# Kernel optimization log

Measured on AMD Instinct MI355X. Metric: run time of the kernel, lower is better.

## Reference

```python
import jax, jax.numpy as jnp
import numpy as np

HS = 1024          # hidden_size
NH_ATTN = 16       # attention heads
NH_LACT = 4        # lact fast-weight heads
DIN = HS // NH_LACT  # 256
DH = DIN             # inter_multi = 1
CHUNK = 1024       # lact_chunk_size
EPS = 1e-5


def setup_inputs() -> dict:
    key = jax.random.key(0)
    ks = jax.random.split(key, 6)
    B, S = 1, 4096
    x = jax.random.normal(ks[0], (B, S, HS), jnp.float32)
    ln_w = jnp.ones((HS,), jnp.float32)
    ln_b = jnp.zeros((HS,), jnp.float32)
    in_proj_w = jax.random.normal(ks[1], (3 * HS, HS), jnp.float32) * (HS ** -0.5)
    in_proj_b = jnp.zeros((3 * HS,), jnp.float32)
    out_proj_w = jax.random.normal(ks[2], (HS, HS), jnp.float32) * (HS ** -0.5)
    out_proj_b = jnp.zeros((HS,), jnp.float32)
    w0 = jax.random.normal(ks[3], (NH_LACT, DH, DIN), jnp.float32) / np.sqrt(DIN)
    w1 = jax.random.normal(ks[4], (NH_LACT, DIN, DH), jnp.float32) / np.sqrt(DH)
    w2 = jax.random.normal(ks[5], (NH_LACT, DH, DIN), jnp.float32) / np.sqrt(DIN)
    return dict(x=x, ln_w=ln_w, ln_b=ln_b, in_proj_w=in_proj_w, in_proj_b=in_proj_b,
                out_proj_w=out_proj_w, out_proj_b=out_proj_b, w0=w0, w1=w1, w2=w2)


def reference(x, ln_w, ln_b, in_proj_w, in_proj_b, out_proj_w, out_proj_b, w0, w1, w2):
    B, S, D = x.shape
    # LayerNorm
    mu = jnp.mean(x, axis=-1, keepdims=True)
    var = jnp.var(x, axis=-1, keepdims=True)
    xn = (x - mu) * jax.lax.rsqrt(var + EPS) * ln_w + ln_b

    # --- torch nn.MultiheadAttention(batch_first=True), self-attention, no mask ---
    qkv = xn @ in_proj_w.T + in_proj_b                      # [B,S,3D]
    q, k, v = jnp.split(qkv, 3, axis=-1)
    hd = D // NH_ATTN
    def heads(t):
        return t.reshape(B, S, NH_ATTN, hd).transpose(0, 2, 1, 3)  # [B,H,S,hd]
    q = heads(q) * (hd ** -0.5)
    k = heads(k)
    v = heads(v)
    attn = jax.nn.softmax(jnp.einsum('bhqd,bhkd->bhqk', q, k), axis=-1)
    ao = jnp.einsum('bhqk,bhkd->bhqd', attn, v).transpose(0, 2, 1, 3).reshape(B, S, D)
    attn_out = ao @ out_proj_w.T + out_proj_b

    # --- chunked fast-weight SwiGLU TTT (block_causal_lact_swiglu) ---
    # q=k=v=chunk; lr0=lr1=lr2=1; each outer chunk is one TTT step starting from
    # the module parameters: update weights on (k,v) then apply to q (block-causal).
    nc = S // CHUNK
    c = xn.reshape(B, nc, CHUNK, NH_LACT, DIN).transpose(0, 1, 3, 2, 4)  # [B,nc,nh,C,din]
    kv = c  # k == v == q == chunk

    # fast-weight SwiGLU forward on keys: f(k) = w1 @ (silu(w0 k) * (w2 k))
    gate = jnp.einsum('bnhcd,hed->bnhce', kv, w0)     # [B,nc,nh,C,dh]
    sg = jax.nn.sigmoid(gate)
    h = gate * sg                                     # silu
    g = jnp.einsum('bnhcd,hed->bnhce', kv, w2)
    hidden = h * g

    # negative dot-product loss L = -sum(v * f(k)) -> dOut = -v
    dout = -kv                                        # [B,nc,nh,C,din]
    dhid = jnp.einsum('bnhcd,hde->bnhce', dout, w1)
    dh = dhid * g
    dg = dhid * h
    dpre = dh * (sg + gate * sg * (1.0 - sg))         # silu'
    dw1 = jnp.einsum('bnhcd,bnhce->bnhde', dout, hidden)
    dw0 = jnp.einsum('bnhce,bnhcd->bnhed', dpre, kv)
    dw2 = jnp.einsum('bnhce,bnhcd->bnhed', dg, kv)

    # SGD step (lr = 1)
    w0n = w0 - dw0   # [B,nc,nh,dh,din]
    w1n = w1 - dw1
    w2n = w2 - dw2

    # apply updated fast weights to queries
    gq = jnp.einsum('bnhcd,bnhed->bnhce', c, w0n)
    hq = gq * jax.nn.sigmoid(gq)
    gq2 = jnp.einsum('bnhcd,bnhed->bnhce', c, w2n)
    oq = jnp.einsum('bnhce,bnhde->bnhcd', hq * gq2, w1n)  # [B,nc,nh,C,din]
    lact_out = oq.transpose(0, 1, 3, 2, 4).reshape(B, S, D)

    return lact_out + attn_out
```

## Files before the change

### kernel.cpp

```cpp
#include <hip/hip_runtime.h>
#include <hip/hip_bf16.h>


typedef __bf16 bf16_t;
typedef __bf16 bf16x8 __attribute__((ext_vector_type(8)));
typedef __bf16 bf16x4 __attribute__((ext_vector_type(4)));
typedef float  f32x4  __attribute__((ext_vector_type(4)));
typedef float  f32x16 __attribute__((ext_vector_type(16)));

#define SW64(r,cg) ((cg) ^ ((r)&7))
#define SW32(r,cg) ((cg) ^ (((r)>>2)&3))

static __device__ __forceinline__ f32x4 mfma16(bf16x8 a, bf16x8 b, f32x4 c){
  return __builtin_amdgcn_mfma_f32_16x16x32_bf16(a, b, c, 0, 0, 0);
}
static __device__ __forceinline__ f32x16 mfma32(bf16x8 a, bf16x8 b, f32x16 c){
  return __builtin_amdgcn_mfma_f32_32x32x16_bf16(a, b, c, 0, 0, 0);
}
__device__ __forceinline__ float sigm(float x){ return 1.0f/(1.0f + __expf(-x)); }
static __device__ __forceinline__ unsigned pkbf(float lo, float hi){
  unsigned short a = __builtin_bit_cast(unsigned short, (__bf16)lo);
  unsigned short b = __builtin_bit_cast(unsigned short, (__bf16)hi);
  return (unsigned)a | ((unsigned)b<<16);
}
static __device__ __forceinline__ float hswap_max(float x){
  float a=x, b=x;
  asm volatile("v_permlane32_swap_b32 %0, %1" : "+v"(a), "+v"(b));
  return fmaxf(a,b);
}
static __device__ __forceinline__ float hswap_add(float x){
  float a=x, b=x;
  asm volatile("v_permlane32_swap_b32 %0, %1" : "+v"(a), "+v"(b));
  return a+b;
}

__global__ __launch_bounds__(256) void ln_kernel(const float* __restrict__ x,
    const float* __restrict__ w, const float* __restrict__ b,
    bf16_t* __restrict__ xnb)
{
  int s = blockIdx.x, t = threadIdx.x;
  const float4* xr = (const float4*)(x + (size_t)s*1024);
  float4 v = xr[t];
  float sum = v.x+v.y+v.z+v.w;
  float ss  = v.x*v.x+v.y*v.y+v.z*v.z+v.w*v.w;
  #pragma unroll
  for (int o=32;o>0;o>>=1){ sum += __shfl_down(sum,o); ss += __shfl_down(ss,o); }
  __shared__ float red[8];
  __shared__ float stats[2];
  int wid=t>>6, lane=t&63;
  if(lane==0){ red[wid]=sum; red[4+wid]=ss; }
  __syncthreads();
  if(t==0){
    float S0=red[0]+red[1]+red[2]+red[3];
    float Q0=red[4]+red[5]+red[6]+red[7];
    float mu=S0*(1.0f/1024.0f);
    float var=Q0*(1.0f/1024.0f)-mu*mu;
    stats[0]=mu; stats[1]=rsqrtf(var+1e-5f);
  }
  __syncthreads();
  float mu=stats[0], rs=stats[1];
  float4 wv=((const float4*)w)[t], bv=((const float4*)b)[t];
  float4 o;
  o.x=(v.x-mu)*rs*wv.x+bv.x;
  o.y=(v.y-mu)*rs*wv.y+bv.y;
  o.z=(v.z-mu)*rs*wv.z+bv.z;
  o.w=(v.w-mu)*rs*wv.w+bv.w;
  bf16x4 ob = { (bf16_t)o.x, (bf16_t)o.y, (bf16_t)o.z, (bf16_t)o.w };
  *(bf16x4*)&xnb[(size_t)s*1024 + t*4] = ob;
}

__global__ __launch_bounds__(256) void prep_weights(
  const float* __restrict__ ipw, const float* __restrict__ opw,
  const float* __restrict__ w0, const float* __restrict__ w2,
  const float* __restrict__ w1,
  bf16_t* __restrict__ ipwb, bf16_t* __restrict__ opwb,
  bf16_t* __restrict__ w0b, bf16_t* __restrict__ w2b, bf16_t* __restrict__ w1tb)
{
  long i = ((long)blockIdx.x*256 + threadIdx.x)*4;
  if (i < 3145728) {
    float4 v = *(const float4*)(ipw + i);
    bf16x4 o = {(bf16_t)v.x,(bf16_t)v.y,(bf16_t)v.z,(bf16_t)v.w};
    *(bf16x4*)&ipwb[i] = o;
  } else if (i < 4194304) {
    long j = i - 3145728;
    float4 v = *(const float4*)(opw + j);
    bf16x4 o = {(bf16_t)v.x,(bf16_t)v.y,(bf16_t)v.z,(bf16_t)v.w};
    *(bf16x4*)&opwb[j] = o;
  } else if (i < 4456448) {
    long j = i - 4194304;
    float4 v = *(const float4*)(w0 + j);
    bf16x4 o = {(bf16_t)v.x,(bf16_t)v.y,(bf16_t)v.z,(bf16_t)v.w};
    *(bf16x4*)&w0b[j] = o;
  } else if (i < 4718592) {
    long j = i - 4456448;
    float4 v = *(const float4*)(w2 + j);
    bf16x4 o = {(bf16_t)v.x,(bf16_t)v.y,(bf16_t)v.z,(bf16_t)v.w};
    *(bf16x4*)&w2b[j] = o;
  } else if (i < 4980736) {
    long j = i - 4718592;
    int h = (int)(j>>16), rem = (int)(j&65535), d = rem>>8, e0 = rem&255;
    float4 v = *(const float4*)(w1 + j);
    bf16_t* dst = w1tb + h*65536 + d;
    dst[(e0+0)*256] = (bf16_t)v.x;
    dst[(e0+1)*256] = (bf16_t)v.y;
    dst[(e0+2)*256] = (bf16_t)v.z;
    dst[(e0+3)*256] = (bf16_t)v.w;
  }
}

__global__ __launch_bounds__(256) void xnT_kernel(const bf16_t* __restrict__ xnb,
                                                  bf16_t* __restrict__ xt)
{
  int dt = blockIdx.x, ct = blockIdx.y, bz = blockIdx.z;
  int nb = bz>>2, hb = bz&3;
  int t = threadIdx.x;
  __shared__ __align__(16) bf16_t T[4096];
  int r = t>>2, seg = t&3;
  const bf16_t* src = xnb + ((size_t)nb*1024 + ct*64 + r)*1024 + hb*256 + dt*64 + seg*16;
  uint4 a0 = *(const uint4*)src;
  uint4 a1 = *(const uint4*)(src + 8);
  *(uint4*)&T[r*64 + ((((seg*2  )&7)^(r&7))<<3)] = a0;
  *(uint4*)&T[r*64 + ((((seg*2+1)&7)^(r&7))<<3)] = a1;
  __syncthreads();
  int d = t>>2, s2 = t&3;
  unsigned uu[8];
  #pragma unroll
  for (int p=0;p<8;p++){
    int c0 = s2*16 + 2*p, c1 = c0+1;
    unsigned short e0 = __builtin_bit_cast(unsigned short,
        T[c0*64 + (((d>>3)^(c0&7))<<3) + (d&7)]);
    unsigned short e1 = __builtin_bit_cast(unsigned short,
        T[c1*64 + (((d>>3)^(c1&7))<<3) + (d&7)]);
    uu[p] = (unsigned)e0 | ((unsigned)e1<<16);
  }
  uint4 o0 = {uu[0],uu[1],uu[2],uu[3]}, o1 = {uu[4],uu[5],uu[6],uu[7]};
  bf16_t* dst = xt + (size_t)bz*262144 + (size_t)(dt*64 + d)*1024 + ct*64 + s2*16;
  *(uint4*)dst = o0;
  *(uint4*)(dst+8) = o1;
}

template<bool AEW>
__device__ __forceinline__ void gemm_core(
    const bf16_t* __restrict__ A, const float* __restrict__ F0,
    const float* __restrict__ F1, int lda,
    const bf16_t* __restrict__ B, int ldb,
    int K, int m0, int n0, f32x4 (&acc)[4][4])
{
  int t = threadIdx.x, l = t&63;
  int w = t>>6, wr = w>>1, wc = w&1;
  __shared__ __align__(16) bf16_t As[4096], Bs[4096];
  int r0 = t>>2, c0 = t&3, r1 = r0+64;
  const bf16_t* Arow0 = nullptr; const bf16_t* Arow1 = nullptr;
  const float *Fa0=nullptr,*Fa1=nullptr,*Fb0=nullptr,*Fb1=nullptr;
  if constexpr (AEW) {
    Fa0 = F0 + (size_t)(m0+r0)*lda + c0*8;
    Fa1 = F0 + (size_t)(m0+r1)*lda + c0*8;
    Fb0 = F1 + (size_t)(m0+r0)*lda + c0*8;
    Fb1 = F1 + (size_t)(m0+r1)*lda + c0*8;
  } else {
    Arow0 = A + (size_t)(m0+r0)*lda + c0*8;
    Arow1 = A + (size_t)(m0+r1)*lda + c0*8;
  }
  const bf16_t* Brow0 = B + (size_t)(n0+r0)*ldb + c0*8;
  const bf16_t* Brow1 = B + (size_t)(n0+r1)*ldb + c0*8;

  uint4 av0, av1, bv0, bv1;
  auto loadA = [&](int k0, uint4& o0, uint4& o1){
    if constexpr (AEW) {
      float4 ga = *(const float4*)(Fa0 + k0), gb = *(const float4*)(Fa0 + k0 + 4);
      float4 ha = *(const float4*)(Fb0 + k0), hb = *(const float4*)(Fb0 + k0 + 4);
      o0.x = pkbf(ga.x*sigm(ga.x)*ha.x, ga.y*sigm(ga.y)*ha.y);
      o0.y = pkbf(ga.z*sigm(ga.z)*ha.z, ga.w*sigm(ga.w)*ha.w);
      o0.z = pkbf(gb.x*sigm(gb.x)*hb.x, gb.y*sigm(gb.y)*hb.y);
      o0.w = pkbf(gb.z*sigm(gb.z)*hb.z, gb.w*sigm(gb.w)*hb.w);
      float4 gc = *(const float4*)(Fa1 + k0), gd = *(const float4*)(Fa1 + k0 + 4);
      float4 hc = *(const float4*)(Fb1 + k0), hd = *(const float4*)(Fb1 + k0 + 4);
      o1.x = pkbf(gc.x*sigm(gc.x)*hc.x, gc.y*sigm(gc.y)*hc.y);
      o1.y = pkbf(gc.z*sigm(gc.z)*hc.z, gc.w*sigm(gc.w)*hc.w);
      o1.z = pkbf(gd.x*sigm(gd.x)*hd.x, gd.y*sigm(gd.y)*hd.y);
      o1.w = pkbf(gd.z*sigm(gd.z)*hd.z, gd.w*sigm(gd.w)*hd.w);
    } else {
      o0 = *(const uint4*)(Arow0 + k0);
      o1 = *(const uint4*)(Arow1 + k0);
    }
  };
  loadA(0, av0, av1);
  bv0 = *(const uint4*)Brow0; bv1 = *(const uint4*)Brow1;
  int wo0 = r0*32 + (SW32(r0,c0)<<3), wo1 = r1*32 + (SW32(r1,c0)<<3);

  for (int k0=0; k0<K; k0+=32) {
    if (k0) __syncthreads();
    *(uint4*)&As[wo0] = av0; *(uint4*)&As[wo1] = av1;
    *(uint4*)&Bs[wo0] = bv0; *(uint4*)&Bs[wo1] = bv1;
    __syncthreads();
    if (k0+32 < K) {
      loadA(k0+32, av0, av1);
      bv0 = *(const uint4*)(Brow0 + k0+32); bv1 = *(const uint4*)(Brow1 + k0+32);
    }
    bf16x8 af[4], bb[4];
    #pragma unroll
    for (int mt=0;mt<4;mt++){
      int row = (wr<<6)+(mt<<4)+(l&15);
      af[mt] = *(bf16x8*)&As[row*32 + (SW32(row, (l>>4))<<3)];
    }
    #pragma unroll
    for (int nt=0;nt<4;nt++){
      int row = (wc<<6)+(nt<<4)+(l&15);
      bb[nt] = *(bf16x8*)&Bs[row*32 + (SW32(row, (l>>4))<<3)];
    }
    #pragma unroll
    for (int mt=0;mt<4;mt++)
      #pragma unroll
      for (int nt=0;nt<4;nt++)
        acc[mt][nt] = mfma16(af[mt], bb[nt], acc[mt][nt]);
  }
}

#define EPILOOP(...) { int l=threadIdx.x&63, w_=threadIdx.x>>6, wr=w_>>1, wc=w_&1; \
  _Pragma("unroll") for(int mt=0;mt<4;mt++) _Pragma("unroll") for(int nt=0;nt<4;nt++) \
  _Pragma("unroll") for(int q=0;q<4;q++){ \
    int gr=m0+(wr<<6)+(mt<<4)+((l>>4)<<2)+q; int gc=n0+(wc<<6)+(nt<<4)+(l&15); \
    float v=acc[mt][nt][q]; __VA_ARGS__ } }

#define ACCZERO f32x4 acc[4][4]; \
  _Pragma("unroll") for(int i_=0;i_<4;i_++) _Pragma("unroll") for(int j_=0;j_<4;j_++){ \
    f32x4 z_={0.f,0.f,0.f,0.f}; acc[i_][j_]=z_; }

template<int EPI>
__global__ __launch_bounds__(256) void gemm_big(
  const bf16_t* __restrict__ A, const bf16_t* __restrict__ B,
  float* __restrict__ C, const float* __restrict__ bias,
  bf16_t* __restrict__ O1, bf16_t* __restrict__ O2, bf16_t* __restrict__ O3,
  int K, int ldc)
{
  int m0 = blockIdx.y<<7, n0 = blockIdx.x<<7;
  ACCZERO
  gemm_core<false>(A, nullptr, nullptr, K, B, K, K, m0, n0, acc);
  EPILOOP(
    if constexpr (EPI==1) {
      C[(size_t)gr*ldc + gc] = v + bias[gc];
    } else {
      v += bias[gc];
      int seg = gc>>10; int c2 = gc&1023; int hh = c2>>6; int dd = c2&63;
      size_t oi = ((size_t)hh*4096 + gr)*64 + dd;
      if (seg==0)      O1[oi] = (bf16_t)(v*0.18033688011112042f);
      else if (seg==1) O2[oi] = (bf16_t)v;
      else             O3[oi] = (bf16_t)v;
    }
  )
}

__global__ __launch_bounds__(256) void lact_fwd(
    const bf16_t* __restrict__ xnb,
    const bf16_t* __restrict__ w0b, const bf16_t* __restrict__ w2b,
    const bf16_t* __restrict__ w1tb,
    float* __restrict__ b0, float* __restrict__ b1, float* __restrict__ b2)
{
  int bz = blockIdx.z, sel = blockIdx.x>>1;
  const bf16_t* A = xnb + (size_t)(bz>>2)*1048576 + (size_t)(bz&3)*256;
  const bf16_t* B = (sel==0?w0b:(sel==1?w2b:w1tb)) + (size_t)(bz&3)*65536;
  float* C = (sel==0?b0:(sel==1?b1:b2)) + (size_t)bz*262144;
  int m0 = blockIdx.y<<7, n0 = (blockIdx.x&1)<<7;
  ACCZERO
  gemm_core<false>(A, nullptr, nullptr, 1024, B, 256, 256, m0, n0, acc);
  EPILOOP( C[(size_t)gr*256 + gc] = v; )
}

__global__ __launch_bounds__(256) void lact_apply(
    const bf16_t* __restrict__ xnb,
    const bf16_t* __restrict__ w0nb, const bf16_t* __restrict__ w2nb,
    float* __restrict__ b0, float* __restrict__ b1)
{
  int bz = blockIdx.z, sel = blockIdx.x>>1;
  const bf16_t* A = xnb + (size_t)(bz>>2)*1048576 + (size_t)(bz&3)*256;
  const bf16_t* B = (sel? w2nb : w0nb) + (size_t)bz*65536;
  float* C = (sel? b1 : b0) + (size_t)bz*262144;
  int m0 = blockIdx.y<<7, n0 = (blockIdx.x&1)<<7;
  ACCZERO
  gemm_core<false>(A, nullptr, nullptr, 1024, B, 256, 256, m0, n0, acc);
  EPILOOP( C[(size_t)gr*256 + gc] = v; )
}

__global__ __launch_bounds__(256) void lact_upd(
    const bf16_t* __restrict__ xnTb, const bf16_t* __restrict__ hTb,
    const bf16_t* __restrict__ pTb,  const bf16_t* __restrict__ gTb,
    const float* __restrict__ w1, const float* __restrict__ w0,
    const float* __restrict__ w2,
    bf16_t* __restrict__ w1nb, bf16_t* __restrict__ w0nb, bf16_t* __restrict__ w2nb)
{
  int zz = blockIdx.z, sub = zz>>4, bz = zz&15, hb = bz&3;
  const bf16_t* A = (sub==0? xnTb : (sub==1? pTb : gTb)) + (size_t)bz*262144;
  const bf16_t* B = (sub==0? hTb : xnTb) + (size_t)bz*262144;
  const float*  P = (sub==0? w1 : (sub==1? w0 : w2)) + (size_t)hb*65536;
  bf16_t*       O = (sub==0? w1nb : (sub==1? w0nb : w2nb)) + (size_t)bz*65536;
  float sgn = (sub==0) ? 1.0f : -1.0f;
  int m0 = blockIdx.y<<7, n0 = blockIdx.x<<7;
  ACCZERO
  gemm_core<false>(A, nullptr, nullptr, 1024, B, 1024, 1024, m0, n0, acc);
  EPILOOP( O[(size_t)gr*256 + gc] = (bf16_t)(P[(size_t)gr*256 + gc] + sgn*v); )
}

__global__ __launch_bounds__(256) void lact_final(
    const float* __restrict__ gq, const float* __restrict__ gq2,
    const bf16_t* __restrict__ w1nb, float* __restrict__ out)
{
  int bz = blockIdx.z;
  const float* F0 = gq  + (size_t)bz*262144;
  const float* F1 = gq2 + (size_t)bz*262144;
  const bf16_t* B = w1nb + (size_t)bz*65536;
  float* C = out + (size_t)(bz>>2)*1048576 + (size_t)(bz&3)*256;
  int m0 = blockIdx.y<<7, n0 = (blockIdx.x&1)<<7;
  ACCZERO
  gemm_core<true>(nullptr, F0, F1, 256, B, 256, 256, m0, n0, acc);
  EPILOOP( C[(size_t)gr*1024 + gc] += v; )
}

__global__ __launch_bounds__(256) void vtrans(const bf16_t* __restrict__ Vb,
                                              bf16_t* __restrict__ Vt)
{
  int st = blockIdx.x, h = blockIdx.y, t = threadIdx.x;
  __shared__ __align__(16) bf16_t T[64*72];
  #pragma unroll
  for (int G=t; G<512; G+=256) {
    int r = G>>3, cg = G&7;
    *(uint4*)&T[r*72 + cg*8] =
      *(const uint4*)(Vb + ((size_t)h*4096 + st*64 + r)*64 + cg*8);
  }
  __syncthreads();
  int d = t>>2, seg = t&3;
  bf16x8 e0, e1;
  #pragma unroll
  for (int i=0;i<8;i++)  e0[i] = T[(seg*16+i)*72 + d];
  #pragma unroll
  for (int i=0;i<8;i++)  e1[i] = T[(seg*16+8+i)*72 + d];
  size_t base = ((size_t)h*64 + d)*4096 + st*64 + seg*16;
  *(bf16x8*)(Vt + base)     = e0;
  *(bf16x8*)(Vt + base + 8) = e1;
}

__global__ __launch_bounds__(256,4) void attn_mfma3(
    const bf16_t* __restrict__ Qb, const bf16_t* __restrict__ Kb,
    const bf16_t* __restrict__ Vt, float* __restrict__ Opart,
    float* __restrict__ mlpart)
{
  int h = blockIdx.x, qblk = blockIdx.y, z = blockIdx.z;
  int t = threadIdx.x, w = t>>6, l = t&63;
  int lh = l>>5, lq = l&31;
  __shared__ __align__(16) bf16_t Ks[4096], Vs[4096];

  const bf16_t* Kg = Kb + (size_t)h*262144 + (size_t)z*131072;
  const bf16_t* Vg = Vt + (size_t)h*262144 + (size_t)z*2048;

  bf16x8 qf[4];
  {
    const bf16_t* Qg = Qb + ((size_t)h*4096 + (size_t)qblk*128 + w*32 + lq)*64 + lh*8;
    #pragma unroll
    for (int s=0;s<4;s++) qf[s] = *(const bf16x8*)(Qg + s*16);
  }

  int r0 = t>>3, c0 = t&7, r1 = r0+32;
  uint4 kv0 = *(const uint4*)(Kg + (size_t)r0*64 + c0*8);
  uint4 kv1 = *(const uint4*)(Kg + (size_t)r1*64 + c0*8);
  uint4 vv0 = *(const uint4*)(Vg + (size_t)r0*4096 + c0*8);
  uint4 vv1 = *(const uint4*)(Vg + (size_t)r1*4096 + c0*8);

  float m_r = -1e30f, l_r = 0.f;
  f32x16 Oa, Ob;
  #pragma unroll
  for (int i=0;i<16;i++){ Oa[i]=0.f; Ob[i]=0.f; }

  int wo0 = r0*64 + (SW64(r0,c0)<<3);
  int wo1 = r1*64 + (SW64(r1,c0)<<3);

  for (int kt=0; kt<32; ++kt) {
    __syncthreads();
    *(uint4*)&Ks[wo0] = kv0;
    *(uint4*)&Ks[wo1] = kv1;
    *(uint4*)&Vs[wo0] = vv0;
    *(uint4*)&Vs[wo1] = vv1;
    __syncthreads();
    if (kt < 31) {
      const bf16_t* Kg2 = Kg + (size_t)(kt+1)*4096;
      kv0 = *(const uint4*)(Kg2 + (size_t)r0*64 + c0*8);
      kv1 = *(const uint4*)(Kg2 + (size_t)r1*64 + c0*8);
      const bf16_t* Vg2 = Vg + (kt+1)*64;
      vv0 = *(const uint4*)(Vg2 + (size_t)r0*4096 + c0*8);
      vv1 = *(const uint4*)(Vg2 + (size_t)r1*4096 + c0*8);
    }
    f32x16 S0, S1;
    #pragma unroll
    for (int i=0;i<16;i++){ S0[i]=0.f; S1[i]=0.f; }
    __builtin_amdgcn_s_setprio(1);
    #pragma unroll
    for (int s=0;s<4;s++){
      int g = (s<<1) + lh;
      bf16x8 k0 = *(const bf16x8*)&Ks[lq*64 + (SW64(lq,g)<<3)];
      int rowb = 32 + lq;
      bf16x8 k1 = *(const bf16x8*)&Ks[rowb*64 + (SW64(rowb,g)<<3)];
      S0 = mfma32(k0, qf[s], S0);
      S1 = mfma32(k1, qf[s], S1);
    }
    __builtin_amdgcn_s_setprio(0);
    float mt_[8];
    #pragma unroll
    for (int i=0;i<8;i++) mt_[i] = fmaxf(fmaxf(S0[i],S0[i+8]), fmaxf(S1[i],S1[i+8]));
    #pragma unroll
    for (int i=0;i<4;i++) mt_[i] = fmaxf(mt_[i], mt_[i+4]);
    float mx = fmaxf(fmaxf(mt_[0],mt_[1]), fmaxf(mt_[2],mt_[3]));
    mx = hswap_max(mx);
    if (__any(mx > m_r + 8.0f)) {
      float mn = fmaxf(m_r, mx);
      float sc = exp2f(m_r - mn);
      l_r *= sc;
      m_r = mn;
      #pragma unroll
      for (int reg=0; reg<16; reg++){
        int row = (reg&3) + 8*(reg>>2) + 4*lh;
        float s_row = __shfl(sc, row);
        Oa[reg] *= s_row;
        Ob[reg] *= s_row;
      }
    }
    #pragma unroll
    for (int i=0;i<16;i++) S0[i] = exp2f(S0[i]-m_r);
    #pragma unroll
    for (int i=0;i<16;i++) S1[i] = exp2f(S1[i]-m_r);
    float rt[8];
    #pragma unroll
    for (int i=0;i<8;i++) rt[i] = (S0[i]+S0[i+8]) + (S1[i]+S1[i+8]);
    #pragma unroll
    for (int i=0;i<4;i++) rt[i] += rt[i+4];
    float rs = (rt[0]+rt[1])+(rt[2]+rt[3]);
    l_r += hswap_add(rs);
    unsigned pk0[4][2], pk1[4][2];
    #pragma unroll
    for (int u2=0; u2<4; u2++){
      #pragma unroll
      for (int wd=0; wd<2; wd++){
        int q0 = 4*u2 + 2*wd;
        pk0[u2][wd] = pkbf(S0[q0], S0[q0+1]);
        pk1[u2][wd] = pkbf(S1[q0], S1[q0+1]);
      }
    }
    __builtin_amdgcn_s_setprio(1);
    #pragma unroll
    for (int ks=0; ks<4; ks++){
      int v0 = 2*(ks&1);
      unsigned x0, x1, y0, y1;
      if (ks < 2) { x0 = pk0[v0][0]; x1 = pk0[v0][1]; y0 = pk0[v0+1][0]; y1 = pk0[v0+1][1]; }
      else        { x0 = pk1[v0][0]; x1 = pk1[v0][1]; y0 = pk1[v0+1][0]; y1 = pk1[v0+1][1]; }
      asm volatile("v_permlane32_swap_b32 %0, %1" : "+v"(x0), "+v"(y0));
      asm volatile("v_permlane32_swap_b32 %0, %1" : "+v"(x1), "+v"(y1));
      uint4 pau = {x0, x1, y0, y1};
      bf16x8 pa = __builtin_bit_cast(bf16x8, pau);
      int g = (ks<<1) + lh;
      bf16x8 vf0 = *(const bf16x8*)&Vs[lq*64 + (SW64(lq,g)<<3)];
      int rowb = 32 + lq;
      bf16x8 vf1 = *(const bf16x8*)&Vs[rowb*64 + (SW64(rowb,g)<<3)];
      Oa = mfma32(pa, vf0, Oa);
      Ob = mfma32(pa, vf1, Ob);
    }
    __builtin_amdgcn_s_setprio(0);
  }
  size_t pb = ((size_t)(h*32+qblk))*2 + z;
  float* Op = Opart + pb*8192 + (size_t)(w*32)*64;
  #pragma unroll
  for (int reg=0; reg<16; reg++){
    int row = (reg&3) + 8*(reg>>2) + 4*lh;
    Op[row*64 + lq]      = Oa[reg];
    Op[row*64 + 32 + lq] = Ob[reg];
  }
  if (l < 32) {
    *(float2*)&mlpart[pb*256 + (size_t)(w*32+l)*2] = float2{m_r, l_r};
  }
}

__global__ __launch_bounds__(256) void attn_merge(
    const float* __restrict__ Opart, const float* __restrict__ mlpart,
    bf16_t* __restrict__ ao)
{
  int h = blockIdx.x, qblk = blockIdx.y, t = threadIdx.x;
  int r = t>>1, ch = (t&1)<<5;
  size_t b = ((size_t)(h*32+qblk))*2;
  const float* O0 = Opart + b*8192;
  const float* O1 = O0 + 8192;
  float2 v0 = ((const float2*)(mlpart + b*256))[r];
  float2 v1 = ((const float2*)(mlpart + b*256 + 256))[r];
  float M = fmaxf(v0.x, v1.x);
  float a0 = exp2f(v0.x - M), a1 = exp2f(v1.x - M);
  float inv = 1.0f/(v0.y*a0 + v1.y*a1);
  float s0 = a0*inv, s1 = a1*inv;
  bf16_t* dst = ao + (size_t)(qblk*128+r)*1024 + h*64 + ch;
  const float* p0 = O0 + r*64 + ch;
  const float* p1 = O1 + r*64 + ch;
  #pragma unroll
  for (int j=0;j<8;j++){
    float4 o0 = *(const float4*)(p0 + j*4);
    float4 o1 = *(const float4*)(p1 + j*4);
    bf16x4 ov;
    ov[0]=(bf16_t)(o0.x*s0+o1.x*s1);
    ov[1]=(bf16_t)(o0.y*s0+o1.y*s1);
    ov[2]=(bf16_t)(o0.z*s0+o1.z*s1);
    ov[3]=(bf16_t)(o0.w*s0+o1.w*s1);
    *(bf16x4*)(dst + j*4) = ov;
  }
}

__global__ __launch_bounds__(256) void ew1T_kernel(
    const float* __restrict__ b0, const float* __restrict__ b1,
    const float* __restrict__ b2,
    bf16_t* __restrict__ hT, bf16_t* __restrict__ pT, bf16_t* __restrict__ gT)
{
  int et = blockIdx.x, ct = blockIdx.y, bz = blockIdx.z;
  int t = threadIdx.x;
  __shared__ __align__(16) bf16_t Th[4096], Tp[4096], Tg[4096];
  int r = t>>2, seg = t&3;
  size_t base = (size_t)bz*262144 + (size_t)(ct*64 + r)*256 + et*64 + seg*16;
  unsigned ph[8], pp[8], pg[8];
  #pragma unroll
  for (int j=0;j<4;j++){
    float4 gate = *(const float4*)(b0 + base + j*4);
    float4 gg   = *(const float4*)(b1 + base + j*4);
    float4 dh   = *(const float4*)(b2 + base + j*4);
    float hid[4], dpre[4], dgv[4];
    #define EW(c,idx) { float sg=sigm(gate.c); float hs=gate.c*sg; hid[idx]=hs*gg.c; \
                        float nd=-dh.c; float dh_=nd*gg.c; \
                        dpre[idx]=dh_*(sg+gate.c*sg*(1.0f-sg)); dgv[idx]=nd*hs; }
    EW(x,0) EW(y,1) EW(z,2) EW(w,3)
    #undef EW
    ph[j*2  ] = pkbf(hid[0],  hid[1]);  ph[j*2+1] = pkbf(hid[2],  hid[3]);
    pp[j*2  ] = pkbf(dpre[0], dpre[1]); pp[j*2+1] = pkbf(dpre[2], dpre[3]);
    pg[j*2  ] = pkbf(dgv[0],  dgv[1]);  pg[j*2+1] = pkbf(dgv[2],  dgv[3]);
  }
  int g0 = ((seg*2  )&7)^(r&7), g1 = ((seg*2+1)&7)^(r&7);
  uint4 h0={ph[0],ph[1],ph[2],ph[3]}, h1={ph[4],ph[5],ph[6],ph[7]};
  uint4 p0={pp[0],pp[1],pp[2],pp[3]}, p1={pp[4],pp[5],pp[6],pp[7]};
  uint4 q0={pg[0],pg[1],pg[2],pg[3]}, q1={pg[4],pg[5],pg[6],pg[7]};
  *(uint4*)&Th[r*64 + (g0<<3)] = h0; *(uint4*)&Th[r*64 + (g1<<3)] = h1;
  *(uint4*)&Tp[r*64 + (g0<<3)] = p0; *(uint4*)&Tp[r*64 + (g1<<3)] = p1;
  *(uint4*)&Tg[r*64 + (g0<<3)] = q0; *(uint4*)&Tg[r*64 + (g1<<3)] = q1;
  __syncthreads();
  int e = t>>2, s2 = t&3;
  size_t obase = (size_t)bz*262144 + (size_t)(et*64 + e)*1024 + ct*64 + s2*16;
  #pragma unroll
  for (int tens=0; tens<3; tens++){
    const bf16_t* T = (tens==0)?Th:(tens==1)?Tp:Tg;
    bf16_t* dst = ((tens==0)?hT:(tens==1)?pT:gT) + obase;
    unsigned uu[8];
    #pragma unroll
    for (int p=0;p<8;p++){
      int c0 = s2*16 + 2*p, c1 = c0+1;
      unsigned short e0 = __builtin_bit_cast(unsigned short,
          T[c0*64 + (((e>>3)^(c0&7))<<3) + (e&7)]);
      unsigned short e1 = __builtin_bit_cast(unsigned short,
          T[c1*64 + (((e>>3)^(c1&7))<<3) + (e&7)]);
      uu[p] = (unsigned)e0 | ((unsigned)e1<<16);
    }
    uint4 o0 = {uu[0],uu[1],uu[2],uu[3]}, o1 = {uu[4],uu[5],uu[6],uu[7]};
    *(uint4*)dst = o0;
    *(uint4*)(dst+8) = o1;
  }
}

extern "C" void kernel_launch(void* const* d_in, const int* in_sizes, int n_in,
                              void* d_out, int out_size, void* d_ws, size_t ws_size,
                              hipStream_t stream) {
  const float* x          = (const float*)d_in[0];
  const float* ln_w       = (const float*)d_in[1];
  const float* ln_b       = (const float*)d_in[2];
  const float* in_proj_w  = (const float*)d_in[3];
  const float* in_proj_b  = (const float*)d_in[4];
  const float* out_proj_w = (const float*)d_in[5];
  const float* out_proj_b = (const float*)d_in[6];
  const float* w0         = (const float*)d_in[7];
  const float* w1         = (const float*)d_in[8];
  const float* w2         = (const float*)d_in[9];
  float* out = (float*)d_out;

  float* ws = (float*)d_ws;
  bf16_t* xnb  = (bf16_t*)(ws);
  bf16_t* Qb   = (bf16_t*)(ws + 2097152);
  bf16_t* Kb   = (bf16_t*)(ws + 4194304);
  float*  buf0 = ws + 6291456;
  float*  buf1 = ws + 10485760;
  float*  buf2 = ws + 14680064;
  bf16_t* xnTb = (bf16_t*)(ws + 18874368);
  bf16_t* hTb  = (bf16_t*)(ws + 20971520);
  bf16_t* pTb  = (bf16_t*)(ws + 23068672);
  bf16_t* gTb  = (bf16_t*)(ws + 25165824);
  float*  Opart= ws + 18874368;
  bf16_t* ipwb = (bf16_t*)(ws + 27262976);
  float*  mlp  = ws + 27262976;
  bf16_t* opwb = (bf16_t*)(ws + 28835840);
  bf16_t* w0b  = (bf16_t*)(ws + 29360128);
  bf16_t* w2b  = (bf16_t*)(ws + 29491200);
  bf16_t* w1tb = (bf16_t*)(ws + 29622272);
  bf16_t* w0nb = (bf16_t*)(ws + 29753344);
  bf16_t* w1nb = (bf16_t*)(ws + 30277632);
  bf16_t* w2nb = (bf16_t*)(ws + 30801920);
  bf16_t* Vb   = (bf16_t*)buf0;
  bf16_t* aob  = (bf16_t*)buf1;
  bf16_t* Vtp  = (bf16_t*)buf2;

  dim3 blk(256);

  ln_kernel<<<dim3(4096),blk,0,stream>>>(x, ln_w, ln_b, xnb);

  prep_weights<<<dim3(4864),blk,0,stream>>>(in_proj_w, out_proj_w, w0, w2, w1,
                                            ipwb, opwb, w0b, w2b, w1tb);

  gemm_big<3><<<dim3(24,32),blk,0,stream>>>(
      xnb, ipwb, nullptr, in_proj_b, Qb, Kb, Vb, 1024, 0);

  vtrans<<<dim3(64,16),blk,0,stream>>>(Vb, Vtp);

  attn_mfma3<<<dim3(16,32,2),blk,0,stream>>>(Qb, Kb, Vtp, Opart, mlp);

  attn_merge<<<dim3(16,32),blk,0,stream>>>(Opart, mlp, aob);

  gemm_big<1><<<dim3(8,32),blk,0,stream>>>(
      aob, opwb, out, out_proj_b, nullptr,nullptr,nullptr, 1024, 1024);

  xnT_kernel<<<dim3(4,16,16),blk,0,stream>>>(xnb, xnTb);

  lact_fwd<<<dim3(6,8,16),blk,0,stream>>>(xnb, w0b, w2b, w1tb, buf0, buf1, buf2);

  ew1T_kernel<<<dim3(4,16,16),blk,0,stream>>>(buf0, buf1, buf2, hTb, pTb, gTb);

  lact_upd<<<dim3(2,2,48),blk,0,stream>>>(xnTb, hTb, pTb, gTb,
                                          w1, w0, w2, w1nb, w0nb, w2nb);

  lact_apply<<<dim3(4,8,16),blk,0,stream>>>(xnb, w0nb, w2nb, buf0, buf1);

  lact_final<<<dim3(2,8,16),blk,0,stream>>>(buf0, buf1, w1nb, out);
}
```

Baseline: 397.1 us.

## Fuse LaCT forward GEMMs with elementwise gradient math and transposed bf16 stores

Replaces the three-output fp32 lact_fwd GEMM plus the separate ew1T transpose kernel with one kernel. Each block computes the w0, w2 and w1t projections for a 128x64 tile in sequence, keeps the first two in packed bf16 registers, then applies the SiLU and gradient math and writes transposed bf16 hT/pT/gT directly. lact_apply likewise fuses silu(gq)*gq2 into a bf16 buffer so lact_final becomes a plain bf16 GEMM. The aim is to cut fp32 intermediate traffic and a kernel launch. In exchange the 64-wide tiles reuse less data per block, the transposed stores are scattered 32-bit writes, and gate/g are now rounded to bf16 before the elementwise math.

```diff
diff --git a/kernel.cpp b/kernel.cpp
--- a/kernel.cpp
+++ b/kernel.cpp
@@ -22,6 +22,12 @@
   unsigned short a = __builtin_bit_cast(unsigned short, (__bf16)lo);
   unsigned short b = __builtin_bit_cast(unsigned short, (__bf16)hi);
   return (unsigned)a | ((unsigned)b<<16);
+}
+static __device__ __forceinline__ float unpk_lo(unsigned u){
+  return (float)__builtin_bit_cast(__bf16,(unsigned short)(u&0xffffu));
+}
+static __device__ __forceinline__ float unpk_hi(unsigned u){
+  return (float)__builtin_bit_cast(__bf16,(unsigned short)(u>>16));
 }
 static __device__ __forceinline__ float hswap_max(float x){
   float a=x, b=x;
@@ -139,10 +145,8 @@
   *(uint4*)(dst+8) = o1;
 }
 
-template<bool AEW>
 __device__ __forceinline__ void gemm_core(
-    const bf16_t* __restrict__ A, const float* __restrict__ F0,
-    const float* __restrict__ F1, int lda,
+    const bf16_t* __restrict__ A, int lda,
     const bf16_t* __restrict__ B, int ldb,
     int K, int m0, int n0, f32x4 (&acc)[4][4])
 {
@@ -150,42 +154,12 @@
   int w = t>>6, wr = w>>1, wc = w&1;
   __shared__ __align__(16) bf16_t As[4096], Bs[4096];
   int r0 = t>>2, c0 = t&3, r1 = r0+64;
-  const bf16_t* Arow0 = nullptr; const bf16_t* Arow1 = nullptr;
-  const float *Fa0=nullptr,*Fa1=nullptr,*Fb0=nullptr,*Fb1=nullptr;
-  if constexpr (AEW) {
-    Fa0 = F0 + (size_t)(m0+r0)*lda + c0*8;
-    Fa1 = F0 + (size_t)(m0+r1)*lda + c0*8;
-    Fb0 = F1 + (size_t)(m0+r0)*lda + c0*8;
-    Fb1 = F1 + (size_t)(m0+r1)*lda + c0*8;
-  } else {
-    Arow0 = A + (size_t)(m0+r0)*lda + c0*8;
-    Arow1 = A + (size_t)(m0+r1)*lda + c0*8;
-  }
+  const bf16_t* Arow0 = A + (size_t)(m0+r0)*lda + c0*8;
+  const bf16_t* Arow1 = A + (size_t)(m0+r1)*lda + c0*8;
   const bf16_t* Brow0 = B + (size_t)(n0+r0)*ldb + c0*8;
   const bf16_t* Brow1 = B + (size_t)(n0+r1)*ldb + c0*8;
-
-  uint4 av0, av1, bv0, bv1;
-  auto loadA = [&](int k0, uint4& o0, uint4& o1){
-    if constexpr (AEW) {
-      float4 ga = *(const float4*)(Fa0 + k0), gb = *(const float4*)(Fa0 + k0 + 4);
-      float4 ha = *(const float4*)(Fb0 + k0), hb = *(const float4*)(Fb0 + k0 + 4);
-      o0.x = pkbf(ga.x*sigm(ga.x)*ha.x, ga.y*sigm(ga.y)*ha.y);
-      o0.y = pkbf(ga.z*sigm(ga.z)*ha.z, ga.w*sigm(ga.w)*ha.w);
-      o0.z = pkbf(gb.x*sigm(gb.x)*hb.x, gb.y*sigm(gb.y)*hb.y);
-      o0.w = pkbf(gb.z*sigm(gb.z)*hb.z, gb.w*sigm(gb.w)*hb.w);
-      float4 gc = *(const float4*)(Fa1 + k0), gd = *(const float4*)(Fa1 + k0 + 4);
-      float4 hc = *(const float4*)(Fb1 + k0), hd = *(const float4*)(Fb1 + k0 + 4);
-      o1.x = pkbf(gc.x*sigm(gc.x)*hc.x, gc.y*sigm(gc.y)*hc.y);
-      o1.y = pkbf(gc.z*sigm(gc.z)*hc.z, gc.w*sigm(gc.w)*hc.w);
-      o1.z = pkbf(gd.x*sigm(gd.x)*hd.x, gd.y*sigm(gd.y)*hd.y);
-      o1.w = pkbf(gd.z*sigm(gd.z)*hd.z, gd.w*sigm(gd.w)*hd.w);
-    } else {
-      o0 = *(const uint4*)(Arow0 + k0);
-      o1 = *(const uint4*)(Arow1 + k0);
-    }
-  };
-  loadA(0, av0, av1);
-  bv0 = *(const uint4*)Brow0; bv1 = *(const uint4*)Brow1;
+  uint4 av0 = *(const uint4*)Arow0, av1 = *(const uint4*)Arow1;
+  uint4 bv0 = *(const uint4*)Brow0, bv1 = *(const uint4*)Brow1;
   int wo0 = r0*32 + (SW32(r0,c0)<<3), wo1 = r1*32 + (SW32(r1,c0)<<3);
 
   for (int k0=0; k0<K; k0+=32) {
@@ -194,7 +168,7 @@
     *(uint4*)&Bs[wo0] = bv0; *(uint4*)&Bs[wo1] = bv1;
     __syncthreads();
     if (k0+32 < K) {
-      loadA(k0+32, av0, av1);
+      av0 = *(const uint4*)(Arow0 + k0+32); av1 = *(const uint4*)(Arow1 + k0+32);
       bv0 = *(const uint4*)(Brow0 + k0+32); bv1 = *(const uint4*)(Brow1 + k0+32);
     }
     bf16x8 af[4], bb[4];
@@ -212,6 +186,50 @@
     for (int mt=0;mt<4;mt++)
       #pragma unroll
       for (int nt=0;nt<4;nt++)
+        acc[mt][nt] = mfma16(af[mt], bb[nt], acc[mt][nt]);
+  }
+}
+
+__device__ __forceinline__ void gemm_core_w(
+    const bf16_t* __restrict__ A, int lda,
+    const bf16_t* __restrict__ B, int ldb,
+    int K, int m0, int n0, f32x4 (&acc)[4][2])
+{
+  int t = threadIdx.x, l = t&63;
+  int w = t>>6, wr = w>>1, wc = w&1;
+  __shared__ __align__(16) bf16_t As[4096], Bs[2048];
+  int r0 = t>>2, c0 = t&3, r1 = r0+64;
+  const bf16_t* Arow0 = A + (size_t)(m0+r0)*lda + c0*8;
+  const bf16_t* Arow1 = A + (size_t)(m0+r1)*lda + c0*8;
+  const bf16_t* Brow  = B + (size_t)(n0+r0)*ldb + c0*8;
+  uint4 av0 = *(const uint4*)Arow0, av1 = *(const uint4*)Arow1;
+  uint4 bv  = *(const uint4*)Brow;
+  int wo0 = r0*32 + (SW32(r0,c0)<<3), wo1 = r1*32 + (SW32(r1,c0)<<3);
+
+  for (int k0=0; k0<K; k0+=32) {
+    if (k0) __syncthreads();
+    *(uint4*)&As[wo0] = av0; *(uint4*)&As[wo1] = av1;
+    *(uint4*)&Bs[wo0] = bv;
+    __syncthreads();
+    if (k0+32 < K) {
+      av0 = *(const uint4*)(Arow0 + k0+32); av1 = *(const uint4*)(Arow1 + k0+32);
+      bv  = *(const uint4*)(Brow + k0+32);
+    }
+    bf16x8 af[4], bb[2];
+    #pragma unroll
+    for (int mt=0;mt<4;mt++){
+      int row = (wr<<6)+(mt<<4)+(l&15);
+      af[mt] = *(bf16x8*)&As[row*32 + (SW32(row, (l>>4))<<3)];
+    }
+    #pragma unroll
+    for (int nt=0;nt<2;nt++){
+      int row = (wc<<5)+(nt<<4)+(l&15);
+      bb[nt] = *(bf16x8*)&Bs[row*32 + (SW32(row, (l>>4))<<3)];
+    }
+    #pragma unroll
+    for (int mt=0;mt<4;mt++)
+      #pragma unroll
+      for (int nt=0;nt<2;nt++)
         acc[mt][nt] = mfma16(af[mt], bb[nt], acc[mt][nt]);
   }
 }
@@ -222,8 +240,12 @@
     int gr=m0+(wr<<6)+(mt<<4)+((l>>4)<<2)+q; int gc=n0+(wc<<6)+(nt<<4)+(l&15); \
     float v=acc[mt][nt][q]; __VA_ARGS__ } }
 
-#define ACCZERO f32x4 acc[4][4]; \
+#define ACCZERO(acc) \
   _Pragma("unroll") for(int i_=0;i_<4;i_++) _Pragma("unroll") for(int j_=0;j_<4;j_++){ \
+    f32x4 z_={0.f,0.f,0.f,0.f}; acc[i_][j_]=z_; }
+
+#define ACCZERO_W(acc) \
+  _Pragma("unroll") for(int i_=0;i_<4;i_++) _Pragma("unroll") for(int j_=0;j_<2;j_++){ \
     f32x4 z_={0.f,0.f,0.f,0.f}; acc[i_][j_]=z_; }
 
 template<int EPI>
@@ -234,8 +256,9 @@
   int K, int ldc)
 {
   int m0 = blockIdx.y<<7, n0 = blockIdx.x<<7;
-  ACCZERO
-  gemm_core<false>(A, nullptr, nullptr, K, B, K, K, m0, n0, acc);
+  f32x4 acc[4][4];
+  ACCZERO(acc)
+  gemm_core(A, K, B, K, K, m0, n0, acc);
   EPILOOP(
     if constexpr (EPI==1) {
       C[(size_t)gr*ldc + gc] = v + bias[gc];
@@ -250,35 +273,111 @@
   )
 }
 
-__global__ __launch_bounds__(256) void lact_fwd(
+__global__ __launch_bounds__(256) void lact_fwd_ew(
     const bf16_t* __restrict__ xnb,
     const bf16_t* __restrict__ w0b, const bf16_t* __restrict__ w2b,
     const bf16_t* __restrict__ w1tb,
-    float* __restrict__ b0, float* __restrict__ b1, float* __restrict__ b2)
-{
-  int bz = blockIdx.z, sel = blockIdx.x>>1;
-  const bf16_t* A = xnb + (size_t)(bz>>2)*1048576 + (size_t)(bz&3)*256;
-  const bf16_t* B = (sel==0?w0b:(sel==1?w2b:w1tb)) + (size_t)(bz&3)*65536;
-  float* C = (sel==0?b0:(sel==1?b1:b2)) + (size_t)bz*262144;
-  int m0 = blockIdx.y<<7, n0 = (blockIdx.x&1)<<7;
-  ACCZERO
-  gemm_core<false>(A, nullptr, nullptr, 1024, B, 256, 256, m0, n0, acc);
-  EPILOOP( C[(size_t)gr*256 + gc] = v; )
-}
-
-__global__ __launch_bounds__(256) void lact_apply(
+    bf16_t* __restrict__ hT, bf16_t* __restrict__ pT, bf16_t* __restrict__ gT)
+{
+  int bz = blockIdx.z, hb = bz&3;
+  const bf16_t* A = xnb + (size_t)(bz>>2)*1048576 + (size_t)hb*256;
+  int m0 = blockIdx.y<<7, n0 = blockIdx.x<<6;
+  f32x4 acc[4][2];
+  unsigned gpk[4][2][2], ppk[4][2][2];
+
+  ACCZERO_W(acc)
+  gemm_core_w(A, 1024, w0b + hb*65536, 256, 256, m0, n0, acc);
+  #pragma unroll
+  for (int mt=0;mt<4;mt++)
+    #pragma unroll
+    for (int nt=0;nt<2;nt++){
+      gpk[mt][nt][0] = pkbf(acc[mt][nt][0], acc[mt][nt][1]);
+      gpk[mt][nt][1] = pkbf(acc[mt][nt][2], acc[mt][nt][3]);
+    }
+  __syncthreads();
+  ACCZERO_W(acc)
+  gemm_core_w(A, 1024, w2b + hb*65536, 256, 256, m0, n0, acc);
+  #pragma unroll
+  for (int mt=0;mt<4;mt++)
+    #pragma unroll
+    for (int nt=0;nt<2;nt++){
+      ppk[mt][nt][0] = pkbf(acc[mt][nt][0], acc[mt][nt][1]);
+      ppk[mt][nt][1] = pkbf(acc[mt][nt][2], acc[mt][nt][3]);
+    }
+  __syncthreads();
+  ACCZERO_W(acc)
+  gemm_core_w(A, 1024, w1tb + hb*65536, 256, 256, m0, n0, acc);
+
+  int l=threadIdx.x&63, w_=threadIdx.x>>6, wr=w_>>1, wc=w_&1;
+  size_t tb = (size_t)bz*262144;
+  #pragma unroll
+  for (int mt=0;mt<4;mt++){
+    #pragma unroll
+    for (int nt=0;nt<2;nt++){
+      int gc = n0 + (wc<<5) + (nt<<4) + (l&15);
+      size_t rowoff = tb + (size_t)gc*1024;
+      #pragma unroll
+      for (int qp=0;qp<2;qp++){
+        int gr0 = m0 + (wr<<6) + (mt<<4) + ((l>>4)<<2) + 2*qp;
+        float gate0 = unpk_lo(gpk[mt][nt][qp]), gate1 = unpk_hi(gpk[mt][nt][qp]);
+        float g0 = unpk_lo(ppk[mt][nt][qp]), g1 = unpk_hi(ppk[mt][nt][qp]);
+        float dh0 = acc[mt][nt][2*qp], dh1 = acc[mt][nt][2*qp+1];
+        float sg0 = sigm(gate0), sg1 = sigm(gate1);
+        float hs0 = gate0*sg0, hs1 = gate1*sg1;
+        float hid0 = hs0*g0, hid1 = hs1*g1;
+        float nd0 = -dh0, nd1 = -dh1;
+        float dpre0 = nd0*g0*(sg0 + gate0*sg0*(1.0f-sg0));
+        float dpre1 = nd1*g1*(sg1 + gate1*sg1*(1.0f-sg1));
+        float dg0 = nd0*hs0, dg1 = nd1*hs1;
+        *(unsigned*)&hT[rowoff + gr0] = pkbf(hid0, hid1);
+        *(unsigned*)&pT[rowoff + gr0] = pkbf(dpre0, dpre1);
+        *(unsigned*)&gT[rowoff + gr0] = pkbf(dg0, dg1);
+      }
+    }
+  }
+}
+
+__global__ __launch_bounds__(256) void lact_apply_u(
     const bf16_t* __restrict__ xnb,
     const bf16_t* __restrict__ w0nb, const bf16_t* __restrict__ w2nb,
-    float* __restrict__ b0, float* __restrict__ b1)
-{
-  int bz = blockIdx.z, sel = blockIdx.x>>1;
+    bf16_t* __restrict__ u)
+{
+  int bz = blockIdx.z;
   const bf16_t* A = xnb + (size_t)(bz>>2)*1048576 + (size_t)(bz&3)*256;
-  const bf16_t* B = (sel? w2nb : w0nb) + (size_t)bz*65536;
-  float* C = (sel? b1 : b0) + (size_t)bz*262144;
-  int m0 = blockIdx.y<<7, n0 = (blockIdx.x&1)<<7;
-  ACCZERO
-  gemm_core<false>(A, nullptr, nullptr, 1024, B, 256, 256, m0, n0, acc);
-  EPILOOP( C[(size_t)gr*256 + gc] = v; )
+  int m0 = blockIdx.y<<7, n0 = blockIdx.x<<6;
+  f32x4 acc[4][2];
+  unsigned qpk[4][2][2];
+
+  ACCZERO_W(acc)
+  gemm_core_w(A, 1024, w2nb + (size_t)bz*65536, 256, 256, m0, n0, acc);
+  #pragma unroll
+  for (int mt=0;mt<4;mt++)
+    #pragma unroll
+    for (int nt=0;nt<2;nt++){
+      qpk[mt][nt][0] = pkbf(acc[mt][nt][0], acc[mt][nt][1]);
+      qpk[mt][nt][1] = pkbf(acc[mt][nt][2], acc[mt][nt][3]);
+    }
+  __syncthreads();
+  ACCZERO_W(acc)
+  gemm_core_w(A, 1024, w0nb + (size_t)bz*65536, 256, 256, m0, n0, acc);
+
+  int l=threadIdx.x&63, w_=threadIdx.x>>6, wr=w_>>1, wc=w_&1;
+  size_t tb = (size_t)bz*262144;
+  #pragma unroll
+  for (int mt=0;mt<4;mt++){
+    #pragma unroll
+    for (int nt=0;nt<2;nt++){
+      int gc = n0 + (wc<<5) + (nt<<4) + (l&15);
+      #pragma unroll
+      for (int qp=0;qp<2;qp++){
+        int gr0 = m0 + (wr<<6) + (mt<<4) + ((l>>4)<<2) + 2*qp;
+        float q20 = unpk_lo(qpk[mt][nt][qp]), q21 = unpk_hi(qpk[mt][nt][qp]);
+        float gq0 = acc[mt][nt][2*qp], gq1 = acc[mt][nt][2*qp+1];
+        u[tb + (size_t)gr0*256 + gc]     = (bf16_t)(gq0*sigm(gq0)*q20);
+        u[tb + (size_t)(gr0+1)*256 + gc] = (bf16_t)(gq1*sigm(gq1)*q21);
+      }
+    }
+  }
 }
 
 __global__ __launch_bounds__(256) void lact_upd(
@@ -295,23 +394,24 @@
   bf16_t*       O = (sub==0? w1nb : (sub==1? w0nb : w2nb)) + (size_t)bz*65536;
   float sgn = (sub==0) ? 1.0f : -1.0f;
   int m0 = blockIdx.y<<7, n0 = blockIdx.x<<7;
-  ACCZERO
-  gemm_core<false>(A, nullptr, nullptr, 1024, B, 1024, 1024, m0, n0, acc);
+  f32x4 acc[4][4];
+  ACCZERO(acc)
+  gemm_core(A, 1024, B, 1024, 1024, m0, n0, acc);
   EPILOOP( O[(size_t)gr*256 + gc] = (bf16_t)(P[(size_t)gr*256 + gc] + sgn*v); )
 }
 
 __global__ __launch_bounds__(256) void lact_final(
-    const float* __restrict__ gq, const float* __restrict__ gq2,
-    const bf16_t* __restrict__ w1nb, float* __restrict__ out)
+    const bf16_t* __restrict__ u, const bf16_t* __restrict__ w1nb,
+    float* __restrict__ out)
 {
   int bz = blockIdx.z;
-  const float* F0 = gq  + (size_t)bz*262144;
-  const float* F1 = gq2 + (size_t)bz*262144;
+  const bf16_t* A = u + (size_t)bz*262144;
   const bf16_t* B = w1nb + (size_t)bz*65536;
   float* C = out + (size_t)(bz>>2)*1048576 + (size_t)(bz&3)*256;
   int m0 = blockIdx.y<<7, n0 = (blockIdx.x&1)<<7;
-  ACCZERO
-  gemm_core<true>(nullptr, F0, F1, 256, B, 256, 256, m0, n0, acc);
+  f32x4 acc[4][4];
+  ACCZERO(acc)
+  gemm_core(A, 256, B, 256, 256, m0, n0, acc);
   EPILOOP( C[(size_t)gr*1024 + gc] += v; )
 }
 
@@ -338,7 +438,8 @@
   *(bf16x8*)(Vt + base + 8) = e1;
 }
 
-__global__ __launch_bounds__(256,4) void attn_mfma3(
+__global__ __launch_bounds__(256)
+__attribute__((amdgpu_waves_per_eu(4,4))) void attn_mfma3(
     const bf16_t* __restrict__ Qb, const bf16_t* __restrict__ Kb,
     const bf16_t* __restrict__ Vt, float* __restrict__ Opart,
     float* __restrict__ mlpart)
@@ -506,62 +607,6 @@
   }
 }
 
-__global__ __launch_bounds__(256) void ew1T_kernel(
-    const float* __restrict__ b0, const float* __restrict__ b1,
-    const float* __restrict__ b2,
-    bf16_t* __restrict__ hT, bf16_t* __restrict__ pT, bf16_t* __restrict__ gT)
-{
-  int et = blockIdx.x, ct = blockIdx.y, bz = blockIdx.z;
-  int t = threadIdx.x;
-  __shared__ __align__(16) bf16_t Th[4096], Tp[4096], Tg[4096];
-  int r = t>>2, seg = t&3;
-  size_t base = (size_t)bz*262144 + (size_t)(ct*64 + r)*256 + et*64 + seg*16;
-  unsigned ph[8], pp[8], pg[8];
-  #pragma unroll
-  for (int j=0;j<4;j++){
-    float4 gate = *(const float4*)(b0 + base + j*4);
-    float4 gg   = *(const float4*)(b1 + base + j*4);
-    float4 dh   = *(const float4*)(b2 + base + j*4);
-    float hid[4], dpre[4], dgv[4];
-    #define EW(c,idx) { float sg=sigm(gate.c); float hs=gate.c*sg; hid[idx]=hs*gg.c; \
-                        float nd=-dh.c; float dh_=nd*gg.c; \
-                        dpre[idx]=dh_*(sg+gate.c*sg*(1.0f-sg)); dgv[idx]=nd*hs; }
-    EW(x,0) EW(y,1) EW(z,2) EW(w,3)
-    #undef EW
-    ph[j*2  ] = pkbf(hid[0],  hid[1]);  ph[j*2+1] = pkbf(hid[2],  hid[3]);
-    pp[j*2  ] = pkbf(dpre[0], dpre[1]); pp[j*2+1] = pkbf(dpre[2], dpre[3]);
-    pg[j*2  ] = pkbf(dgv[0],  dgv[1]);  pg[j*2+1] = pkbf(dgv[2],  dgv[3]);
-  }
-  int g0 = ((seg*2  )&7)^(r&7), g1 = ((seg*2+1)&7)^(r&7);
-  uint4 h0={ph[0],ph[1],ph[2],ph[3]}, h1={ph[4],ph[5],ph[6],ph[7]};
-  uint4 p0={pp[0],pp[1],pp[2],pp[3]}, p1={pp[4],pp[5],pp[6],pp[7]};
-  uint4 q0={pg[0],pg[1],pg[2],pg[3]}, q1={pg[4],pg[5],pg[6],pg[7]};
-  *(uint4*)&Th[r*64 + (g0<<3)] = h0; *(uint4*)&Th[r*64 + (g1<<3)] = h1;
-  *(uint4*)&Tp[r*64 + (g0<<3)] = p0; *(uint4*)&Tp[r*64 + (g1<<3)] = p1;
-  *(uint4*)&Tg[r*64 + (g0<<3)] = q0; *(uint4*)&Tg[r*64 + (g1<<3)] = q1;
-  __syncthreads();
-  int e = t>>2, s2 = t&3;
-  size_t obase = (size_t)bz*262144 + (size_t)(et*64 + e)*1024 + ct*64 + s2*16;
-  #pragma unroll
-  for (int tens=0; tens<3; tens++){
-    const bf16_t* T = (tens==0)?Th:(tens==1)?Tp:Tg;
-    bf16_t* dst = ((tens==0)?hT:(tens==1)?pT:gT) + obase;
-    unsigned uu[8];
-    #pragma unroll
-    for (int p=0;p<8;p++){
-      int c0 = s2*16 + 2*p, c1 = c0+1;
-      unsigned short e0 = __builtin_bit_cast(unsigned short,
-          T[c0*64 + (((e>>3)^(c0&7))<<3) + (e&7)]);
-      unsigned short e1 = __builtin_bit_cast(unsigned short,
-          T[c1*64 + (((e>>3)^(c1&7))<<3) + (e&7)]);
-      uu[p] = (unsigned)e0 | ((unsigned)e1<<16);
-    }
-    uint4 o0 = {uu[0],uu[1],uu[2],uu[3]}, o1 = {uu[4],uu[5],uu[6],uu[7]};
-    *(uint4*)dst = o0;
-    *(uint4*)(dst+8) = o1;
-  }
-}
-
 extern "C" void kernel_launch(void* const* d_in, const int* in_sizes, int n_in,
                               void* d_out, int out_size, void* d_ws, size_t ws_size,
                               hipStream_t stream) {
@@ -581,9 +626,10 @@
   bf16_t* xnb  = (bf16_t*)(ws);
   bf16_t* Qb   = (bf16_t*)(ws + 2097152);
   bf16_t* Kb   = (bf16_t*)(ws + 4194304);
-  float*  buf0 = ws + 6291456;
-  float*  buf1 = ws + 10485760;
-  float*  buf2 = ws + 14680064;
+  bf16_t* Vb   = (bf16_t*)(ws + 6291456);
+  bf16_t* ub   = (bf16_t*)(ws + 6291456);
+  bf16_t* aob  = (bf16_t*)(ws + 10485760);
+  bf16_t* Vtp  = (bf16_t*)(ws + 14680064);
   bf16_t* xnTb = (bf16_t*)(ws + 18874368);
   bf16_t* hTb  = (bf16_t*)(ws + 20971520);
   bf16_t* pTb  = (bf16_t*)(ws + 23068672);
@@ -598,9 +644,6 @@
   bf16_t* w0nb = (bf16_t*)(ws + 29753344);
   bf16_t* w1nb = (bf16_t*)(ws + 30277632);
   bf16_t* w2nb = (bf16_t*)(ws + 30801920);
-  bf16_t* Vb   = (bf16_t*)buf0;
-  bf16_t* aob  = (bf16_t*)buf1;
-  bf16_t* Vtp  = (bf16_t*)buf2;
 
   dim3 blk(256);
 
@@ -623,14 +666,12 @@
 
   xnT_kernel<<<dim3(4,16,16),blk,0,stream>>>(xnb, xnTb);
 
-  lact_fwd<<<dim3(6,8,16),blk,0,stream>>>(xnb, w0b, w2b, w1tb, buf0, buf1, buf2);
-
-  ew1T_kernel<<<dim3(4,16,16),blk,0,stream>>>(buf0, buf1, buf2, hTb, pTb, gTb);
+  lact_fwd_ew<<<dim3(4,8,16),blk,0,stream>>>(xnb, w0b, w2b, w1tb, hTb, pTb, gTb);
 
   lact_upd<<<dim3(2,2,48),blk,0,stream>>>(xnTb, hTb, pTb, gTb,
                                           w1, w0, w2, w1nb, w0nb, w2nb);
 
-  lact_apply<<<dim3(4,8,16),blk,0,stream>>>(xnb, w0nb, w2nb, buf0, buf1);
-
-  lact_final<<<dim3(2,8,16),blk,0,stream>>>(buf0, buf1, w1nb, out);
-}
+  lact_apply_u<<<dim3(4,8,16),blk,0,stream>>>(xnb, w0nb, w2nb, ub);
+
+  lact_final<<<dim3(2,8,16),blk,0,stream>>>(ub, w1nb, out);
+}
```

After: 387.1 us. 2.5% less time.
